# Kernel tuning notes

Hardware: AMD Instinct MI355X
Metric: run time of the kernel (lower is better)

## Reference

```python
import jax, jax.numpy as jnp
import numpy as np

C = 256      # channels (multiple of 32 for GroupNorm)
K = 3        # kernel
PAD = 1      # padding
G = 32       # GroupNorm groups
EPS = 1e-5


def setup_inputs() -> dict:
    key = jax.random.key(0)
    ks = jax.random.split(key, 7)
    B, H, W = 4, 64, 64
    return {
        "x": jax.random.normal(ks[0], (B, C, H, W), jnp.float32),
        "offset": jax.random.normal(ks[1], (B, 2 * K * K, H, W), jnp.float32),
        "weight": jax.random.normal(ks[2], (C, C, K, K), jnp.float32) * 0.01,
        "att_w": jax.random.normal(ks[3], (1, C), jnp.float32) * 0.01,
        "att_b": jnp.zeros((1,), jnp.float32),
        "gamma": jnp.ones((C,), jnp.float32),
        "beta": jnp.zeros((C,), jnp.float32),
    }


def _bilinear_one(xb, py, px):
    # xb: [C, H, W]; py, px: [KK, H, W] fractional sample coords (zero-pad outside)
    H, W = xb.shape[1], xb.shape[2]
    y0 = jnp.floor(py)
    x0 = jnp.floor(px)
    y1 = y0 + 1.0
    x1 = x0 + 1.0
    wy1 = py - y0
    wy0 = 1.0 - wy1
    wx1 = px - x0
    wx0 = 1.0 - wx1

    def g(yi, xi):
        valid = (yi >= 0) & (yi < H) & (xi >= 0) & (xi < W)
        yc = jnp.clip(yi, 0, H - 1).astype(jnp.int32)
        xc = jnp.clip(xi, 0, W - 1).astype(jnp.int32)
        return xb[:, yc, xc] * valid[None].astype(xb.dtype)  # [C, KK, H, W]

    return (g(y0, x0) * (wy0 * wx0)[None] + g(y0, x1) * (wy0 * wx1)[None]
            + g(y1, x0) * (wy1 * wx0)[None] + g(y1, x1) * (wy1 * wx1)[None])


def reference(x, offset, weight, att_w, att_b, gamma, beta):
    B, Cc, H, W = x.shape
    KK = K * K
    off = offset.reshape(B, KK, 2, H, W)  # (dy, dx) per kernel tap
    ii, jj = jnp.meshgrid(jnp.arange(K), jnp.arange(K), indexing='ij')
    dky = (ii - PAD).reshape(KK).astype(x.dtype)
    dkx = (jj - PAD).reshape(KK).astype(x.dtype)
    ys = jnp.arange(H, dtype=x.dtype)
    xs = jnp.arange(W, dtype=x.dtype)
    # sample coords [B, KK, H, W]
    py = ys[None, :, None] + dky[:, None, None] + off[:, :, 0]
    px = xs[None, None, :] + dkx[:, None, None] + off[:, :, 1]

    # deformable unfold: [B, C, KK, H, W]
    xu = jax.vmap(_bilinear_one)(x, py, px)

    # max over kernel taps -> channel attention gate
    xm = xu.max(axis=2)  # [B, C, H, W]
    att = jax.nn.sigmoid(jnp.einsum('bchw,oc->bohw', xm, att_w)
                         + att_b[None, :, None, None])  # [B, 1, H, W]

    # gate the unfolded samples, then emulate the conv as one GEMM
    xw = xu * att[:, :, None]  # broadcast over C, KK
    cols = xw.transpose(1, 2, 0, 3, 4).reshape(Cc * KK, B * H * W)  # [C*KK, BHW]
    out = (weight.reshape(Cc, Cc * KK) @ cols).reshape(Cc, B, H, W).transpose(1, 0, 2, 3)

    # GroupNorm(32, C) + ReLU
    og = out.reshape(B, G, Cc // G, H, W)
    mu = og.mean(axis=(2, 3, 4), keepdims=True)
    var = og.var(axis=(2, 3, 4), keepdims=True)
    on = ((og - mu) * jax.lax.rsqrt(var + EPS)).reshape(B, Cc, H, W)
    return jax.nn.relu(on * gamma[None, :, None, None] + beta[None, :, None, None])
```

## Files before the change

### kernel.cpp

```cpp
#include <hip/hip_runtime.h>

#define CT 256
#define KDIM 2304
#define ROUNDS 8
#define COLP 296

typedef unsigned short u16;
typedef __attribute__((ext_vector_type(8))) short bf16x8;
typedef __attribute__((ext_vector_type(4))) float f32x4;

__device__ __forceinline__ unsigned f2b(float f) {
    unsigned u = __float_as_uint(f);
    u += 0x7fffu + ((u >> 16) & 1u);
    return u >> 16;
}
__device__ __forceinline__ float lo_bf(unsigned u) { return __uint_as_float(u << 16); }
__device__ __forceinline__ float hi_bf(unsigned u) { return __uint_as_float(u & 0xffff0000u); }

__global__ __launch_bounds__(256) void k_prep(const float* __restrict__ x, uint4* __restrict__ xi,
                                              const float* __restrict__ wgt, uint4* __restrict__ pw)
{
    if (blockIdx.x < 2048) {
        int u = blockIdx.x * 256 + threadIdx.x;
        int bcg = u >> 12, p = u & 4095;
        const float* xp = x + (((size_t)bcg) << 15) + p;
        unsigned r[4];
#pragma unroll
        for (int i = 0; i < 4; ++i) {
            float a = xp[(size_t)(2 * i) << 12];
            float c = xp[(size_t)(2 * i + 1) << 12];
            r[i] = f2b(a) | (f2b(c) << 16);
        }
        uint4 o; o.x = r[0]; o.y = r[1]; o.z = r[2]; o.w = r[3];
        xi[u] = o;
    } else {
        int u = (blockIdx.x - 2048) * 256 + threadIdx.x;
        int kc = u >> 10, rm = u & 1023;
        int m = rm >> 2, j = rm & 3;
        int round = kc / 9, tap = kc - round * 9;
        const float* src = wgt + (size_t)m * KDIM + tap;
        int c0 = round * 32 + j * 8;
        unsigned q[4];
#pragma unroll
        for (int i = 0; i < 4; ++i) {
            float a = src[(size_t)(c0 + 2 * i) * 9];
            float c = src[(size_t)(c0 + 2 * i + 1) * 9];
            q[i] = f2b(a) | (f2b(c) << 16);
        }
        uint4 o; o.x = q[0]; o.y = q[1]; o.z = q[2]; o.w = q[3];
        pw[u] = o;
    }
}

__global__ __launch_bounds__(512, 2) void k_main(const uint4* __restrict__ xi, const float* __restrict__ off,
                                                 const uint4* __restrict__ pw, const float* __restrict__ att_w,
                                                 const float* __restrict__ att_b,
                                                 float* __restrict__ outp, float* __restrict__ gnpart)
{
    __shared__ float4 s_wt[288];
    __shared__ int2 s_off[288];
    __shared__ u16 Xs[7680];
    __shared__ u16 col[32 * COLP];
    __shared__ float s_att[32];

    int rowblk = blockIdx.x >> 1, half = blockIdx.x & 1;
    int b = rowblk >> 6, h = rowblk & 63, n0 = half * 32;
    int tid = threadIdx.x;
    int lane = tid & 63, w = tid >> 6;
    int l15 = lane & 15, kb = lane >> 4;
    int wm = w * 32;

    for (int e = tid; e < 288; e += 512) {
        int kk = e >> 5, wl = e & 31;
        int ww_ = n0 + wl;
        int ky = kk / 3, kx = kk - ky * 3;
        float dy = off[((size_t)(b * 18 + 2 * kk) * 64 + h) * 64 + ww_];
        float dx = off[((size_t)(b * 18 + 2 * kk + 1) * 64 + h) * 64 + ww_];
        float py = (float)(h + ky - 1) + dy;
        float px = (float)(ww_ + kx - 1) + dx;
        float y0f = floorf(py), x0f = floorf(px);
        int y0 = (int)y0f, x0 = (int)x0f;
        float fy = py - y0f, fx = px - x0f;
        float vy0 = (y0 >= 0 && y0 < 64) ? 1.f : 0.f;
        float vy1 = (y0 >= -1 && y0 < 63) ? 1.f : 0.f;
        float vx0 = (x0 >= 0 && x0 < 64) ? 1.f : 0.f;
        float vx1 = (x0 >= -1 && x0 < 63) ? 1.f : 0.f;
        float4 wt;
        wt.x = (1.f - fy) * (1.f - fx) * vy0 * vx0;
        wt.y = (1.f - fy) * fx * vy0 * vx1;
        wt.z = fy * (1.f - fx) * vy1 * vx0;
        wt.w = fy * fx * vy1 * vx1;
        int yc0 = min(max(y0, 0), 63), yc1 = min(max(y0 + 1, 0), 63);
        int xc0 = min(max(x0, 0), 63), xc1 = min(max(x0 + 1, 0), 63);
        s_wt[e] = wt;
        s_off[e] = make_int2((yc0 * 64 + xc0) | ((yc0 * 64 + xc1) << 16),
                             (yc1 * 64 + xc0) | ((yc1 * 64 + xc1) << 16));
    }

    int r0 = max(0, h - 7), r1 = min(63, h + 7);
    int nrows = r1 - r0 + 1, nw = nrows * 64, rbase = r0 * 64;

    float att_acc = 0.f;
    f32x4 acc[2][2];
#pragma unroll
    for (int mt = 0; mt < 2; ++mt)
#pragma unroll
        for (int nt = 0; nt < 2; ++nt) acc[mt][nt] = (f32x4){0.f, 0.f, 0.f, 0.f};

    for (int round = 0; round < ROUNDS; ++round) {
        for (int sp = 0; sp < 4; ++sp) {
            int cg = round * 4 + sp;
            size_t xibase = (size_t)(b * 32 + cg) << 12;
            __syncthreads();
            for (int u2 = tid; u2 < nrows * 64; u2 += 512)
                ((uint4*)Xs)[u2] = xi[xibase + rbase + u2];
            __syncthreads();
            for (int it = tid; it < 288; it += 512) {
                int tap = it >> 5, nn = it & 31;
                float4 wt = s_wt[it];
                int2 of = s_off[it];
                int P00 = of.x & 0xffff, P01 = (of.x >> 16) & 0xffff;
                int P10 = of.y & 0xffff, P11 = (of.y >> 16) & 0xffff;
                uint4 c00, c01, c10, c11;
                int Q;
                Q = P00 - rbase;
                if ((unsigned)Q < (unsigned)nw) c00 = *(const uint4*)&Xs[Q * 8]; else c00 = xi[xibase + P00];
                Q = P01 - rbase;
                if ((unsigned)Q < (unsigned)nw) c01 = *(const uint4*)&Xs[Q * 8]; else c01 = xi[xibase + P01];
                Q = P10 - rbase;
                if ((unsigned)Q < (unsigned)nw) c10 = *(const uint4*)&Xs[Q * 8]; else c10 = xi[xibase + P10];
                Q = P11 - rbase;
                if ((unsigned)Q < (unsigned)nw) c11 = *(const uint4*)&Xs[Q * 8]; else c11 = xi[xibase + P11];
                const unsigned* a00 = (const unsigned*)&c00;
                const unsigned* a01 = (const unsigned*)&c01;
                const unsigned* a10 = (const unsigned*)&c10;
                const unsigned* a11 = (const unsigned*)&c11;
                unsigned o[4];
#pragma unroll
                for (int q = 0; q < 4; ++q) {
                    float v0 = wt.x * lo_bf(a00[q]) + wt.y * lo_bf(a01[q]) + wt.z * lo_bf(a10[q]) + wt.w * lo_bf(a11[q]);
                    float v1 = wt.x * hi_bf(a00[q]) + wt.y * hi_bf(a01[q]) + wt.z * hi_bf(a10[q]) + wt.w * hi_bf(a11[q]);
                    o[q] = f2b(v0) | (f2b(v1) << 16);
                }
                uint4 ov; ov.x = o[0]; ov.y = o[1]; ov.z = o[2]; ov.w = o[3];
                *(uint4*)&col[nn * COLP + tap * 32 + sp * 8] = ov;
            }
        }
        __syncthreads();

        if (tid < 64) {
            int nn = tid >> 1, h2 = tid & 1;
#pragma unroll
            for (int sp = 0; sp < 4; ++sp) {
                const u16* base = &col[nn * COLP + sp * 8 + h2 * 4];
                float m0 = -1e30f, m1 = -1e30f, m2 = -1e30f, m3 = -1e30f;
#pragma unroll
                for (int t = 0; t < 9; ++t) {
                    uint2 v = *(const uint2*)(base + t * 32);
                    m0 = fmaxf(m0, lo_bf(v.x)); m1 = fmaxf(m1, hi_bf(v.x));
                    m2 = fmaxf(m2, lo_bf(v.y)); m3 = fmaxf(m3, hi_bf(v.y));
                }
                int cb = round * 32 + sp * 8 + h2 * 4;
                att_acc += att_w[cb] * m0 + att_w[cb + 1] * m1 + att_w[cb + 2] * m2 + att_w[cb + 3] * m3;
            }
        }

#pragma unroll
        for (int ts = 0; ts < 9; ++ts) {
            int kc = round * 9 + ts;
            bf16x8 bf[2];
#pragma unroll
            for (int nt = 0; nt < 2; ++nt)
                bf[nt] = *(const bf16x8*)&col[(nt * 16 + l15) * COLP + ts * 32 + kb * 8];
#pragma unroll
            for (int mt = 0; mt < 2; ++mt) {
                uint4 a = pw[(size_t)kc * 1024 + (wm + mt * 16 + l15) * 4 + kb];
                bf16x8 af = __builtin_bit_cast(bf16x8, a);
#pragma unroll
                for (int nt = 0; nt < 2; ++nt)
                    acc[mt][nt] = __builtin_amdgcn_mfma_f32_16x16x32_bf16(af, bf[nt], acc[mt][nt], 0, 0, 0);
            }
        }
    }

    if (tid < 64) {
        float v = att_acc + __shfl_xor(att_acc, 1);
        if ((tid & 1) == 0) s_att[tid >> 1] = 1.f / (1.f + expf(-(v + att_b[0])));
    }
    __syncthreads();

    float attn[2];
#pragma unroll
    for (int nt = 0; nt < 2; ++nt) attn[nt] = s_att[nt * 16 + l15];

#pragma unroll
    for (int mt = 0; mt < 2; ++mt) {
        float s1 = 0.f, s2 = 0.f;
#pragma unroll
        for (int nt = 0; nt < 2; ++nt)
#pragma unroll
            for (int r = 0; r < 4; ++r) {
                float v = acc[mt][nt][r] * attn[nt];
                int m = wm + mt * 16 + kb * 4 + r;
                outp[(((size_t)(b * CT + m)) << 12) + h * 64 + n0 + nt * 16 + l15] = v;
                s1 += v; s2 += v * v;
            }
#pragma unroll
        for (int d = 1; d <= 16; d <<= 1) {
            s1 += __shfl_xor(s1, d);
            s2 += __shfl_xor(s2, d);
        }
        if ((lane & 31) == 0) {
            int gidx = w * 4 + mt * 2 + (kb >> 1);
            gnpart[blockIdx.x * 64 + gidx * 2] = s1;
            gnpart[blockIdx.x * 64 + gidx * 2 + 1] = s2;
        }
    }
}

__global__ __launch_bounds__(256) void k_gn(const float* __restrict__ gnpart, const float* __restrict__ gamma,
                                            const float* __restrict__ beta, float* __restrict__ outp)
{
    __shared__ float rs1[128], rs2[128];
    __shared__ float s_stat[2];
    int bg = blockIdx.x;
    int b = bg >> 5, g = bg & 31;
    int tid = threadIdx.x;
    if (tid < 128) {
        int blk = (b * 64 + (tid >> 1)) * 2 + (tid & 1);
        rs1[tid] = gnpart[blk * 64 + g * 2];
        rs2[tid] = gnpart[blk * 64 + g * 2 + 1];
    }
    __syncthreads();
    if (tid < 64) {
        float a = rs1[tid] + rs1[tid + 64];
        float c = rs2[tid] + rs2[tid + 64];
#pragma unroll
        for (int d = 1; d <= 32; d <<= 1) {
            a += __shfl_xor(a, d);
            c += __shfl_xor(c, d);
        }
        if (tid == 0) {
            float mean = a * (1.f / 32768.f);
            float var = c * (1.f / 32768.f) - mean * mean;
            s_stat[0] = mean;
            s_stat[1] = rsqrtf(var + 1e-5f);
        }
    }
    __syncthreads();
    float mean = s_stat[0], rstd = s_stat[1];
    float4* p4 = (float4*)(outp + ((size_t)(b * CT + g * 8) << 12));
    for (int i = tid; i < 8192; i += 256) {
        int c = g * 8 + (i >> 10);
        float ga = gamma[c], be = beta[c];
        float4 v = p4[i];
        float4 r;
        r.x = fmaxf((v.x - mean) * rstd * ga + be, 0.f);
        r.y = fmaxf((v.y - mean) * rstd * ga + be, 0.f);
        r.z = fmaxf((v.z - mean) * rstd * ga + be, 0.f);
        r.w = fmaxf((v.w - mean) * rstd * ga + be, 0.f);
        p4[i] = r;
    }
}

extern "C" void kernel_launch(void* const* d_in, const int* in_sizes, int n_in,
                              void* d_out, int out_size, void* d_ws, size_t ws_size,
                              hipStream_t stream)
{
    const float* x = (const float*)d_in[0];
    const float* off = (const float*)d_in[1];
    const float* wgt = (const float*)d_in[2];
    const float* attw = (const float*)d_in[3];
    const float* attb = (const float*)d_in[4];
    const float* gamma = (const float*)d_in[5];
    const float* beta = (const float*)d_in[6];
    float* outp = (float*)d_out;

    char* ws = (char*)d_ws;
    uint4* xi = (uint4*)ws;
    uint4* pw = (uint4*)(ws + 8388608);
    float* gnpart = (float*)(ws + 9568256);

    k_prep<<<dim3(2336), dim3(256), 0, stream>>>(x, xi, wgt, pw);
    k_main<<<dim3(512), dim3(512), 0, stream>>>(xi, off, pw, attw, attb, outp, gnpart);
    k_gn<<<dim3(128), dim3(256), 0, stream>>>(gnpart, gamma, beta, outp);
}
```

Measured before the change: 167.2 us.

## Split GEMM reduction across two blocks and move attention gating into GroupNorm kernel

```diff
diff --git a/kernel.cpp b/kernel.cpp
--- a/kernel.cpp
+++ b/kernel.cpp
@@ -2,12 +2,12 @@
 
 #define CT 256
 #define KDIM 2304
-#define ROUNDS 8
 #define COLP 296
 
 typedef unsigned short u16;
 typedef __attribute__((ext_vector_type(8))) short bf16x8;
 typedef __attribute__((ext_vector_type(4))) float f32x4;
+typedef __fp16 fp16x2 __attribute__((ext_vector_type(2)));
 
 __device__ __forceinline__ unsigned f2b(float f) {
     unsigned u = __float_as_uint(f);
@@ -52,19 +52,21 @@
     }
 }
 
-__global__ __launch_bounds__(512, 2) void k_main(const uint4* __restrict__ xi, const float* __restrict__ off,
+__global__ __launch_bounds__(512, 8) void k_main(const uint4* __restrict__ xi, const float* __restrict__ off,
                                                  const uint4* __restrict__ pw, const float* __restrict__ att_w,
-                                                 const float* __restrict__ att_b,
-                                                 float* __restrict__ outp, float* __restrict__ gnpart)
+                                                 float* __restrict__ pout0, float* __restrict__ pout1,
+                                                 float* __restrict__ ap0, float* __restrict__ ap1)
 {
-    __shared__ float4 s_wt[288];
+    __shared__ uint2 s_wt[288];
     __shared__ int2 s_off[288];
     __shared__ u16 Xs[7680];
     __shared__ u16 col[32 * COLP];
-    __shared__ float s_att[32];
-
-    int rowblk = blockIdx.x >> 1, half = blockIdx.x & 1;
+
+    int bx = blockIdx.x;
+    int rowblk = bx >> 2, half = (bx >> 1) & 1, khalf = bx & 1;
     int b = rowblk >> 6, h = rowblk & 63, n0 = half * 32;
+    float* pout = khalf ? pout1 : pout0;
+    float* ap = khalf ? ap1 : ap0;
     int tid = threadIdx.x;
     int lane = tid & 63, w = tid >> 6;
     int l15 = lane & 15, kb = lane >> 4;
@@ -85,14 +87,18 @@
         float vy1 = (y0 >= -1 && y0 < 63) ? 1.f : 0.f;
         float vx0 = (x0 >= 0 && x0 < 64) ? 1.f : 0.f;
         float vx1 = (x0 >= -1 && x0 < 63) ? 1.f : 0.f;
-        float4 wt;
-        wt.x = (1.f - fy) * (1.f - fx) * vy0 * vx0;
-        wt.y = (1.f - fy) * fx * vy0 * vx1;
-        wt.z = fy * (1.f - fx) * vy1 * vx0;
-        wt.w = fy * fx * vy1 * vx1;
+        float w0 = (1.f - fy) * (1.f - fx) * vy0 * vx0;
+        float w1 = (1.f - fy) * fx * vy0 * vx1;
+        float w2 = fy * (1.f - fx) * vy1 * vx0;
+        float w3 = fy * fx * vy1 * vx1;
+        fp16x2 pA = __builtin_amdgcn_cvt_pkrtz(w0, w1);
+        fp16x2 pB = __builtin_amdgcn_cvt_pkrtz(w2, w3);
+        uint2 wp;
+        wp.x = __builtin_bit_cast(unsigned, pA);
+        wp.y = __builtin_bit_cast(unsigned, pB);
         int yc0 = min(max(y0, 0), 63), yc1 = min(max(y0 + 1, 0), 63);
         int xc0 = min(max(x0, 0), 63), xc1 = min(max(x0 + 1, 0), 63);
-        s_wt[e] = wt;
+        s_wt[e] = wp;
         s_off[e] = make_int2((yc0 * 64 + xc0) | ((yc0 * 64 + xc1) << 16),
                              (yc1 * 64 + xc0) | ((yc1 * 64 + xc1) << 16));
     }
@@ -107,7 +113,8 @@
 #pragma unroll
         for (int nt = 0; nt < 2; ++nt) acc[mt][nt] = (f32x4){0.f, 0.f, 0.f, 0.f};
 
-    for (int round = 0; round < ROUNDS; ++round) {
+    for (int rr = 0; rr < 4; ++rr) {
+        int round = khalf * 4 + rr;
         for (int sp = 0; sp < 4; ++sp) {
             int cg = round * 4 + sp;
             size_t xibase = (size_t)(b * 32 + cg) << 12;
@@ -117,7 +124,11 @@
             __syncthreads();
             for (int it = tid; it < 288; it += 512) {
                 int tap = it >> 5, nn = it & 31;
-                float4 wt = s_wt[it];
+                uint2 wp = s_wt[it];
+                fp16x2 wA = __builtin_bit_cast(fp16x2, wp.x);
+                fp16x2 wB = __builtin_bit_cast(fp16x2, wp.y);
+                float wx = (float)wA[0], wy = (float)wA[1];
+                float wz = (float)wB[0], ww2 = (float)wB[1];
                 int2 of = s_off[it];
                 int P00 = of.x & 0xffff, P01 = (of.x >> 16) & 0xffff;
                 int P10 = of.y & 0xffff, P11 = (of.y >> 16) & 0xffff;
@@ -138,8 +149,8 @@
                 unsigned o[4];
 #pragma unroll
                 for (int q = 0; q < 4; ++q) {
-                    float v0 = wt.x * lo_bf(a00[q]) + wt.y * lo_bf(a01[q]) + wt.z * lo_bf(a10[q]) + wt.w * lo_bf(a11[q]);
-                    float v1 = wt.x * hi_bf(a00[q]) + wt.y * hi_bf(a01[q]) + wt.z * hi_bf(a10[q]) + wt.w * hi_bf(a11[q]);
+                    float v0 = wx * lo_bf(a00[q]) + wy * lo_bf(a01[q]) + wz * lo_bf(a10[q]) + ww2 * lo_bf(a11[q]);
+                    float v1 = wx * hi_bf(a00[q]) + wy * hi_bf(a01[q]) + wz * hi_bf(a10[q]) + ww2 * hi_bf(a11[q]);
                     o[q] = f2b(v0) | (f2b(v1) << 16);
                 }
                 uint4 ov; ov.x = o[0]; ov.y = o[1]; ov.z = o[2]; ov.w = o[3];
@@ -185,81 +196,81 @@
 
     if (tid < 64) {
         float v = att_acc + __shfl_xor(att_acc, 1);
-        if ((tid & 1) == 0) s_att[tid >> 1] = 1.f / (1.f + expf(-(v + att_b[0])));
-    }
-    __syncthreads();
-
-    float attn[2];
-#pragma unroll
-    for (int nt = 0; nt < 2; ++nt) attn[nt] = s_att[nt * 16 + l15];
-
-#pragma unroll
-    for (int mt = 0; mt < 2; ++mt) {
-        float s1 = 0.f, s2 = 0.f;
+        if ((tid & 1) == 0) ap[rowblk * 64 + n0 + (tid >> 1)] = v;
+    }
+
+#pragma unroll
+    for (int mt = 0; mt < 2; ++mt)
 #pragma unroll
         for (int nt = 0; nt < 2; ++nt)
 #pragma unroll
             for (int r = 0; r < 4; ++r) {
-                float v = acc[mt][nt][r] * attn[nt];
                 int m = wm + mt * 16 + kb * 4 + r;
-                outp[(((size_t)(b * CT + m)) << 12) + h * 64 + n0 + nt * 16 + l15] = v;
-                s1 += v; s2 += v * v;
+                pout[(((size_t)(b * CT + m)) << 12) + h * 64 + n0 + nt * 16 + l15] = acc[mt][nt][r];
             }
-#pragma unroll
-        for (int d = 1; d <= 16; d <<= 1) {
-            s1 += __shfl_xor(s1, d);
-            s2 += __shfl_xor(s2, d);
-        }
-        if ((lane & 31) == 0) {
-            int gidx = w * 4 + mt * 2 + (kb >> 1);
-            gnpart[blockIdx.x * 64 + gidx * 2] = s1;
-            gnpart[blockIdx.x * 64 + gidx * 2 + 1] = s2;
-        }
-    }
-}
-
-__global__ __launch_bounds__(256) void k_gn(const float* __restrict__ gnpart, const float* __restrict__ gamma,
+}
+
+__global__ __launch_bounds__(256) void k_gn(const float* __restrict__ p0, const float* __restrict__ p1,
+                                            const float* __restrict__ ap0, const float* __restrict__ ap1,
+                                            const float* __restrict__ att_b, const float* __restrict__ gamma,
                                             const float* __restrict__ beta, float* __restrict__ outp)
 {
-    __shared__ float rs1[128], rs2[128];
-    __shared__ float s_stat[2];
-    int bg = blockIdx.x;
-    int b = bg >> 5, g = bg & 31;
+    __shared__ float s_att[4096];
+    __shared__ float rs1[4], rs2[4], s_stat[2];
+    int bg = blockIdx.x, b = bg >> 5, g = bg & 31;
     int tid = threadIdx.x;
-    if (tid < 128) {
-        int blk = (b * 64 + (tid >> 1)) * 2 + (tid & 1);
-        rs1[tid] = gnpart[blk * 64 + g * 2];
-        rs2[tid] = gnpart[blk * 64 + g * 2 + 1];
+    float ab = att_b[0];
+    for (int i = tid; i < 4096; i += 256) {
+        float s = ab + ap0[b * 4096 + i] + ap1[b * 4096 + i];
+        s_att[i] = 1.f / (1.f + expf(-s));
     }
     __syncthreads();
-    if (tid < 64) {
-        float a = rs1[tid] + rs1[tid + 64];
-        float c = rs2[tid] + rs2[tid + 64];
-#pragma unroll
-        for (int d = 1; d <= 32; d <<= 1) {
-            a += __shfl_xor(a, d);
-            c += __shfl_xor(c, d);
-        }
-        if (tid == 0) {
-            float mean = a * (1.f / 32768.f);
-            float var = c * (1.f / 32768.f) - mean * mean;
-            s_stat[0] = mean;
-            s_stat[1] = rsqrtf(var + 1e-5f);
-        }
+
+    size_t base4 = ((size_t)(b * CT + g * 8) << 12) >> 2;
+    const float4* q0 = (const float4*)p0;
+    const float4* q1 = (const float4*)p1;
+    float4* o4 = (float4*)outp;
+    float s1 = 0.f, s2 = 0.f;
+    for (int i = tid; i < 8192; i += 256) {
+        int pos4 = i & 1023;
+        float4 a = q0[base4 + i], c = q1[base4 + i];
+        float4 t = *(const float4*)&s_att[pos4 * 4];
+        float4 v;
+        v.x = (a.x + c.x) * t.x;
+        v.y = (a.y + c.y) * t.y;
+        v.z = (a.z + c.z) * t.z;
+        v.w = (a.w + c.w) * t.w;
+        o4[base4 + i] = v;
+        s1 += (v.x + v.y) + (v.z + v.w);
+        s2 += v.x * v.x + v.y * v.y + v.z * v.z + v.w * v.w;
+    }
+#pragma unroll
+    for (int d = 1; d <= 32; d <<= 1) {
+        s1 += __shfl_xor(s1, d);
+        s2 += __shfl_xor(s2, d);
+    }
+    if ((tid & 63) == 0) { rs1[tid >> 6] = s1; rs2[tid >> 6] = s2; }
+    __syncthreads();
+    if (tid == 0) {
+        float S1 = rs1[0] + rs1[1] + rs1[2] + rs1[3];
+        float S2 = rs2[0] + rs2[1] + rs2[2] + rs2[3];
+        float mean = S1 * (1.f / 32768.f);
+        float var = S2 * (1.f / 32768.f) - mean * mean;
+        s_stat[0] = mean;
+        s_stat[1] = rsqrtf(var + 1e-5f);
     }
     __syncthreads();
     float mean = s_stat[0], rstd = s_stat[1];
-    float4* p4 = (float4*)(outp + ((size_t)(b * CT + g * 8) << 12));
     for (int i = tid; i < 8192; i += 256) {
         int c = g * 8 + (i >> 10);
         float ga = gamma[c], be = beta[c];
-        float4 v = p4[i];
+        float4 v = o4[base4 + i];
         float4 r;
         r.x = fmaxf((v.x - mean) * rstd * ga + be, 0.f);
         r.y = fmaxf((v.y - mean) * rstd * ga + be, 0.f);
         r.z = fmaxf((v.z - mean) * rstd * ga + be, 0.f);
         r.w = fmaxf((v.w - mean) * rstd * ga + be, 0.f);
-        p4[i] = r;
+        o4[base4 + i] = r;
     }
 }
 
@@ -279,9 +290,12 @@
     char* ws = (char*)d_ws;
     uint4* xi = (uint4*)ws;
     uint4* pw = (uint4*)(ws + 8388608);
-    float* gnpart = (float*)(ws + 9568256);
+    float* pout0 = (float*)(ws + 9568256);
+    float* pout1 = (float*)(ws + 26345472);
+    float* ap0 = (float*)(ws + 43122688);
+    float* ap1 = (float*)(ws + 43188224);
 
     k_prep<<<dim3(2336), dim3(256), 0, stream>>>(x, xi, wgt, pw);
-    k_main<<<dim3(512), dim3(512), 0, stream>>>(xi, off, pw, attw, attb, outp, gnpart);
-    k_gn<<<dim3(128), dim3(256), 0, stream>>>(gnpart, gamma, beta, outp);
-}
+    k_main<<<dim3(1024), dim3(512), 0, stream>>>(xi, off, pw, attw, pout0, pout1, ap0, ap1);
+    k_gn<<<dim3(128), dim3(256), 0, stream>>>(pout0, pout1, ap0, ap1, attb, gamma, beta, outp);
+}
```

Measured after the change: 188.9 us. +13.0%, slower.

## Process two channel groups per stage with register-prefetched next-stage slab

Applied to the files above, without the earlier changes.

```diff
diff --git a/kernel.cpp b/kernel.cpp
--- a/kernel.cpp
+++ b/kernel.cpp
@@ -2,12 +2,12 @@
 
 #define CT 256
 #define KDIM 2304
-#define ROUNDS 8
 #define COLP 296
 
 typedef unsigned short u16;
 typedef __attribute__((ext_vector_type(8))) short bf16x8;
 typedef __attribute__((ext_vector_type(4))) float f32x4;
+typedef __fp16 fp16x2 __attribute__((ext_vector_type(2)));
 
 __device__ __forceinline__ unsigned f2b(float f) {
     unsigned u = __float_as_uint(f);
@@ -57,9 +57,9 @@
                                                  const float* __restrict__ att_b,
                                                  float* __restrict__ outp, float* __restrict__ gnpart)
 {
-    __shared__ float4 s_wt[288];
+    __shared__ uint2 s_wt[288];
     __shared__ int2 s_off[288];
-    __shared__ u16 Xs[7680];
+    __shared__ u16 Xs[2 * 7680];
     __shared__ u16 col[32 * COLP];
     __shared__ float s_att[32];
 
@@ -85,20 +85,26 @@
         float vy1 = (y0 >= -1 && y0 < 63) ? 1.f : 0.f;
         float vx0 = (x0 >= 0 && x0 < 64) ? 1.f : 0.f;
         float vx1 = (x0 >= -1 && x0 < 63) ? 1.f : 0.f;
-        float4 wt;
-        wt.x = (1.f - fy) * (1.f - fx) * vy0 * vx0;
-        wt.y = (1.f - fy) * fx * vy0 * vx1;
-        wt.z = fy * (1.f - fx) * vy1 * vx0;
-        wt.w = fy * fx * vy1 * vx1;
+        float w0 = (1.f - fy) * (1.f - fx) * vy0 * vx0;
+        float w1 = (1.f - fy) * fx * vy0 * vx1;
+        float w2 = fy * (1.f - fx) * vy1 * vx0;
+        float w3 = fy * fx * vy1 * vx1;
+        fp16x2 pA = __builtin_amdgcn_cvt_pkrtz(w0, w1);
+        fp16x2 pB = __builtin_amdgcn_cvt_pkrtz(w2, w3);
+        uint2 wp;
+        wp.x = __builtin_bit_cast(unsigned, pA);
+        wp.y = __builtin_bit_cast(unsigned, pB);
         int yc0 = min(max(y0, 0), 63), yc1 = min(max(y0 + 1, 0), 63);
         int xc0 = min(max(x0, 0), 63), xc1 = min(max(x0 + 1, 0), 63);
-        s_wt[e] = wt;
+        s_wt[e] = wp;
         s_off[e] = make_int2((yc0 * 64 + xc0) | ((yc0 * 64 + xc1) << 16),
                              (yc1 * 64 + xc0) | ((yc1 * 64 + xc1) << 16));
     }
 
     int r0 = max(0, h - 7), r1 = min(63, h + 7);
     int nrows = r1 - r0 + 1, nw = nrows * 64, rbase = r0 * 64;
+    int nw2 = nw * 2;
+    size_t xib = (size_t)(b * 32) << 12;
 
     float att_acc = 0.f;
     f32x4 acc[2][2];
@@ -107,30 +113,58 @@
 #pragma unroll
         for (int nt = 0; nt < 2; ++nt) acc[mt][nt] = (f32x4){0.f, 0.f, 0.f, 0.f};
 
-    for (int round = 0; round < ROUNDS; ++round) {
-        for (int sp = 0; sp < 4; ++sp) {
-            int cg = round * 4 + sp;
-            size_t xibase = (size_t)(b * 32 + cg) << 12;
+    uint4 pf[4];
+#pragma unroll
+    for (int i = 0; i < 4; ++i) {
+        int e = tid + i * 512;
+        int cgl = (e >= nw) ? 1 : 0;
+        int idx = e - cgl * nw;
+        if (e < nw2) pf[i] = xi[xib + ((size_t)cgl << 12) + rbase + idx];
+    }
+
+    for (int round = 0; round < 8; ++round) {
+        for (int s2 = 0; s2 < 2; ++s2) {
+            int stage = round * 2 + s2;
             __syncthreads();
-            for (int u2 = tid; u2 < nrows * 64; u2 += 512)
-                ((uint4*)Xs)[u2] = xi[xibase + rbase + u2];
+#pragma unroll
+            for (int i = 0; i < 4; ++i) {
+                int e = tid + i * 512;
+                if (e < nw2) ((uint4*)Xs)[e] = pf[i];
+            }
             __syncthreads();
-            for (int it = tid; it < 288; it += 512) {
-                int tap = it >> 5, nn = it & 31;
-                float4 wt = s_wt[it];
-                int2 of = s_off[it];
+            int ns = min(stage + 1, 15);
+            size_t nb0 = xib + ((size_t)(ns * 2) << 12) + rbase;
+#pragma unroll
+            for (int i = 0; i < 4; ++i) {
+                int e = tid + i * 512;
+                int cgl = (e >= nw) ? 1 : 0;
+                int idx = e - cgl * nw;
+                if (e < nw2) pf[i] = xi[nb0 + ((size_t)cgl << 12) + idx];
+            }
+            for (int it = tid; it < 576; it += 512) {
+                int cgl = (it >= 288) ? 1 : 0;
+                int it2 = it - cgl * 288;
+                int tap = it2 >> 5, nn = it2 & 31;
+                int xsb = cgl * nw * 8;
+                size_t gfall = xib + ((size_t)(stage * 2 + cgl) << 12);
+                uint2 wp = s_wt[it2];
+                fp16x2 wA = __builtin_bit_cast(fp16x2, wp.x);
+                fp16x2 wB = __builtin_bit_cast(fp16x2, wp.y);
+                float wx = (float)wA[0], wy = (float)wA[1];
+                float wz = (float)wB[0], ww2 = (float)wB[1];
+                int2 of = s_off[it2];
                 int P00 = of.x & 0xffff, P01 = (of.x >> 16) & 0xffff;
                 int P10 = of.y & 0xffff, P11 = (of.y >> 16) & 0xffff;
                 uint4 c00, c01, c10, c11;
                 int Q;
                 Q = P00 - rbase;
-                if ((unsigned)Q < (unsigned)nw) c00 = *(const uint4*)&Xs[Q * 8]; else c00 = xi[xibase + P00];
+                if ((unsigned)Q < (unsigned)nw) c00 = *(const uint4*)&Xs[xsb + Q * 8]; else c00 = xi[gfall + P00];
                 Q = P01 - rbase;
-                if ((unsigned)Q < (unsigned)nw) c01 = *(const uint4*)&Xs[Q * 8]; else c01 = xi[xibase + P01];
+                if ((unsigned)Q < (unsigned)nw) c01 = *(const uint4*)&Xs[xsb + Q * 8]; else c01 = xi[gfall + P01];
                 Q = P10 - rbase;
-                if ((unsigned)Q < (unsigned)nw) c10 = *(const uint4*)&Xs[Q * 8]; else c10 = xi[xibase + P10];
+                if ((unsigned)Q < (unsigned)nw) c10 = *(const uint4*)&Xs[xsb + Q * 8]; else c10 = xi[gfall + P10];
                 Q = P11 - rbase;
-                if ((unsigned)Q < (unsigned)nw) c11 = *(const uint4*)&Xs[Q * 8]; else c11 = xi[xibase + P11];
+                if ((unsigned)Q < (unsigned)nw) c11 = *(const uint4*)&Xs[xsb + Q * 8]; else c11 = xi[gfall + P11];
                 const unsigned* a00 = (const unsigned*)&c00;
                 const unsigned* a01 = (const unsigned*)&c01;
                 const unsigned* a10 = (const unsigned*)&c10;
@@ -138,11 +172,12 @@
                 unsigned o[4];
 #pragma unroll
                 for (int q = 0; q < 4; ++q) {
-                    float v0 = wt.x * lo_bf(a00[q]) + wt.y * lo_bf(a01[q]) + wt.z * lo_bf(a10[q]) + wt.w * lo_bf(a11[q]);
-                    float v1 = wt.x * hi_bf(a00[q]) + wt.y * hi_bf(a01[q]) + wt.z * hi_bf(a10[q]) + wt.w * hi_bf(a11[q]);
+                    float v0 = wx * lo_bf(a00[q]) + wy * lo_bf(a01[q]) + wz * lo_bf(a10[q]) + ww2 * lo_bf(a11[q]);
+                    float v1 = wx * hi_bf(a00[q]) + wy * hi_bf(a01[q]) + wz * hi_bf(a10[q]) + ww2 * hi_bf(a11[q]);
                     o[q] = f2b(v0) | (f2b(v1) << 16);
                 }
                 uint4 ov; ov.x = o[0]; ov.y = o[1]; ov.z = o[2]; ov.w = o[3];
+                int sp = s2 * 2 + cgl;
                 *(uint4*)&col[nn * COLP + tap * 32 + sp * 8] = ov;
             }
         }
```

Measured after the change: 204.0 us. +22.0%, slower.
